# Optimization experiments

Measured on AMD Instinct MI355X. Metric: run time of the kernel, lower is better.

## Reference

```python
import jax, jax.numpy as jnp
import numpy as np

SIGMAS = [0.5, 1.0, 2.0, 4.0, 8.0]
FILTER_SIZE = int(4 * SIGMAS[-1] + 1)  # 33
PAD = int(2 * SIGMAS[-1])              # 16
K1, K2 = 0.01, 0.03
ALPHA = 0.025
COMPENSATION = 20.0
DATA_RANGE = 1.0


def _gauss_2d(size, sigma):
    coords = np.arange(size, dtype=np.float32) - size // 2
    g = np.exp(-coords ** 2 / (2.0 * sigma ** 2))
    g = g / g.sum()
    return np.outer(g, g)


def _build_g_masks():
    # [n_sigmas, 1, 33, 33] OIHW
    masks = np.stack([_gauss_2d(FILTER_SIZE, s)[None] for s in SIGMAS], axis=0)
    return jnp.asarray(masks, dtype=jnp.float32)


def setup_inputs() -> dict:
    key = jax.random.key(0)
    kx, ky = jax.random.split(key)
    x = jax.random.uniform(kx, (16, 1, 512, 512), dtype=jnp.float32)
    y = jax.random.uniform(ky, (16, 1, 512, 512), dtype=jnp.float32)
    return {"x": x, "y": y, "g_masks": _build_g_masks()}


def _conv(t, w):
    # t: [B,1,H,W], w: [O,1,33,33] -> [B,O,H,W] ('same' padding)
    return jax.lax.conv_general_dilated(
        t, w, window_strides=(1, 1), padding=[(PAD, PAD), (PAD, PAD)],
        dimension_numbers=("NCHW", "OIHW", "NCHW"))


def reference(x, y, g_masks):
    C1 = (K1 * DATA_RANGE) ** 2
    C2 = (K2 * DATA_RANGE) ** 2

    mux = _conv(x, g_masks)   # [B,5,H,W]
    muy = _conv(y, g_masks)
    mux2 = mux * mux
    muy2 = muy * muy
    muxy = mux * muy
    sigmax2 = _conv(x * x, g_masks) - mux2
    sigmay2 = _conv(y * y, g_masks) - muy2
    sigmaxy = _conv(x * y, g_masks) - muxy

    luminance = (2.0 * muxy + C1) / (mux2 + muy2 + C1)
    cs = (2.0 * sigmaxy + C2) / (sigmax2 + sigmay2 + C2)

    lM = luminance[:, -1, :, :]          # largest-scale luminance
    PIcs = jnp.prod(cs, axis=1)          # product of contrast-structure over scales
    loss_ms_ssim = 1.0 - lM * PIcs       # [B,H,W]

    loss_l1 = jnp.abs(x - y)             # [B,1,H,W]
    gaussian_l1 = _conv(loss_l1, g_masks[-1:]).mean(axis=1)  # [B,H,W]

    loss_mix = ALPHA * loss_ms_ssim + (1.0 - ALPHA) * gaussian_l1 / DATA_RANGE
    return (COMPENSATION * loss_mix).mean()
```

## Files before the change

kernel.cpp:

```cpp
#include <hip/hip_runtime.h>
#include <hip/hip_bf16.h>

namespace {

constexpr float kAlpha = 0.025f;
constexpr float kC1 = 1.0e-4f;
constexpr float kC2 = 9.0e-4f;

constexpr int MPS = 72;
constexpr int HTS = 72;

typedef __attribute__((ext_vector_type(8))) short short8;
typedef __attribute__((ext_vector_type(4))) float f32x4;

struct __align__(16) Smem {
  union {
    short mp[2][64 * MPS];
    short hbT[4][32 * HTS];
  };
  float red[4];
  int gtab[2][5][48];
};

union Frag {
  int i[4];
  int4 i4;
  short8 s8;
};

__device__ __forceinline__ unsigned f2bf(float f) {
  unsigned u = __float_as_uint(f);
  return (u + 0x7FFFu + ((u >> 16) & 1u)) >> 16;
}
__device__ __forceinline__ unsigned pk(float a, float b) {
  union {
    __hip_bfloat162 h;
    unsigned u;
  } c;
  c.h = __float22bfloat162_rn(make_float2(a, b));
  return c.u;
}
__device__ __forceinline__ float bfl(unsigned u) {
  return __uint_as_float(u << 16);
}
__device__ __forceinline__ float bfh(unsigned u) {
  return __uint_as_float(u & 0xFFFF0000u);
}
__device__ __forceinline__ float frcp(float x) {
  return __builtin_amdgcn_rcpf(x);
}

__device__ __forceinline__ short8 wbuild2(const int* tb, int nt, int kt) {
  Frag u;
#pragma unroll
  for (int j = 0; j < 4; ++j) u.i[j] = tb[16 * kt - 8 * nt + 8 + j];
  return u.s8;
}

__device__ __forceinline__ void load_xy(const Smem& sm, int row, int quad,
                                        Frag fx[2], Frag fy[2]) {
  const short* px = &sm.mp[0][row * MPS + quad * 8];
  const short* py = &sm.mp[1][row * MPS + quad * 8];
  fx[0].i4 = *(const int4*)(px);
  fx[1].i4 = *(const int4*)(px + 32);
  fy[0].i4 = *(const int4*)(py);
  fy[1].i4 = *(const int4*)(py + 32);
}

template <bool USE_WS>
__global__ __launch_bounds__(256, 4) void msssim_l1_kernel(
    const float* __restrict__ x, const float* __restrict__ y,
    const float* __restrict__ gm, float* __restrict__ partial,
    float* __restrict__ out) {
  __shared__ Smem sm;
  const int tid = threadIdx.x;
  const int lane = tid & 63;
  const int w = tid >> 6;
  const int quad = lane >> 4;
  const int l16 = lane & 15;
  const f32x4 kZ = {0.f, 0.f, 0.f, 0.f};

  float corr;
  {
    float traw4 = (lane < 33) ? gm[4 * 1089 + 528 + lane] : 0.f;
    float g = traw4 * rsqrtf(__shfl(traw4, 16, 64));
    float se = g, st = bfl(f2bf(g));
#pragma unroll
    for (int off = 32; off > 0; off >>= 1) {
      se += __shfl_xor(se, off, 64);
      st += __shfl_xor(st, off, 64);
    }
    float r1 = se / st;
    corr = r1 * r1;
  }

  {
    int* gt = &sm.gtab[0][0][0];
    for (int q = tid; q < 480; q += 256) {
      int par = q >= 240;
      int rem = par ? q - 240 : q;
      int s = rem / 48;
      int i = rem - s * 48;
      int t0 = 2 * i + par;
      const float* grow = gm + s * 1089 + 528;
      float rsc = rsqrtf(grow[16]);
      int g0 = t0 - 31, g1 = t0 - 30;
      unsigned lo = (g0 >= 0 && g0 <= 32) ? f2bf(grow[g0] * rsc) : 0u;
      unsigned hi = (g1 >= 0 && g1 <= 32) ? f2bf(grow[g1] * rsc) : 0u;
      gt[q] = (int)(lo | (hi << 16));
    }
  }

  const int D = (quad * 8 - l16 + 31) >> 1;
  const int* gD = &sm.gtab[(l16 & 1) ? 0 : 1][0][0] + D - 8;

  const float* xb = x + blockIdx.z * (512 * 512);
  const float* yb = y + blockIdx.z * (512 * 512);
  const int rb = blockIdx.y * 32 - 16;
  const int cb = blockIdx.x * 32 - 16;
  for (int f = tid; f < 1024; f += 256) {
    int pr = f >> 4;
    int pc = (f & 15) << 2;
    int gr = rb + pr, gc = cb + pc;
    float4 vx = make_float4(0.f, 0.f, 0.f, 0.f);
    float4 vy = vx;
    if (gr >= 0 && gr < 512 && gc >= 0 && gc < 512) {
      vx = *(const float4*)(xb + gr * 512 + gc);
      vy = *(const float4*)(yb + gr * 512 + gc);
    }
    const int base = pr * MPS + pc;
    *(int2*)(&sm.mp[0][base]) =
        make_int2((int)pk(vx.x, vx.y), (int)pk(vx.z, vx.w));
    *(int2*)(&sm.mp[1][base]) =
        make_int2((int)pk(vy.x, vy.y), (int)pk(vy.z, vy.w));
  }
  __syncthreads();

  Frag A[4][2];
  Frag dA[2];
#pragma unroll
  for (int mt = 0; mt < 4; ++mt) {
    Frag fx[2], fy[2];
    load_xy(sm, mt * 16 + l16, quad, fx, fy);
    if (mt == w) {
#pragma unroll
      for (int h = 0; h < 2; ++h)
#pragma unroll
        for (int i = 0; i < 4; ++i) {
          unsigned ux = (unsigned)fx[h].i[i], uy = (unsigned)fy[h].i[i];
          dA[h].i[i] =
              (int)pk(fabsf(bfl(ux) - bfl(uy)), fabsf(bfh(ux) - bfh(uy)));
        }
    }
    if (w == 0) {
      A[mt][0] = fx[0];
      A[mt][1] = fx[1];
    } else if (w == 1) {
      A[mt][0] = fy[0];
      A[mt][1] = fy[1];
    } else {
#pragma unroll
      for (int h = 0; h < 2; ++h)
#pragma unroll
        for (int i = 0; i < 4; ++i) {
          unsigned ux = (unsigned)fx[h].i[i], uy = (unsigned)fy[h].i[i];
          float xl = bfl(ux), xh = bfh(ux), yl = bfl(uy), yh = bfh(uy);
          A[mt][h].i[i] = (w == 2) ? (int)pk(fmaf(xl, xl, yl * yl),
                                            fmaf(xh, xh, yh * yh))
                                   : (int)pk(xl * yl, xh * yh);
        }
    }
  }

  int2 l1h[2];
  {
    const int* tb = gD + 4 * 48;
#pragma unroll
    for (int nt = 0; nt < 2; ++nt) {
      short8 w0 = wbuild2(tb, nt, 0);
      short8 w1 = wbuild2(tb, nt, 1);
      f32x4 acc = __builtin_amdgcn_mfma_f32_16x16x32_bf16(dA[0].s8, w0, kZ, 0,
                                                          0, 0);
      acc = __builtin_amdgcn_mfma_f32_16x16x32_bf16(dA[1].s8, w1, acc, 0, 0,
                                                    0);
      l1h[nt] = make_int2((int)pk(acc[0], acc[1]), (int)pk(acc[2], acc[3]));
    }
  }
  __syncthreads();

  const int mtv = w >> 1, ntv = w & 1;
  f32x4 Pcs = {1.f, 1.f, 1.f, 1.f};
  f32x4 lumP = {0.f, 0.f, 0.f, 0.f};
  f32x4 l1v = {0.f, 0.f, 0.f, 0.f};

#pragma unroll
  for (int s = 0; s < 5; ++s) {
    const int* tb = gD + s * 48;
#pragma unroll
    for (int nt = 0; nt < 2; ++nt) {
      short8 w0 = wbuild2(tb, nt, 0);
      short8 w1 = wbuild2(tb, nt, 1);
#pragma unroll
      for (int mt = 0; mt < 4; ++mt) {
        f32x4 acc = __builtin_amdgcn_mfma_f32_16x16x32_bf16(A[mt][0].s8, w0,
                                                            kZ, 0, 0, 0);
        acc = __builtin_amdgcn_mfma_f32_16x16x32_bf16(A[mt][1].s8, w1, acc, 0,
                                                      0, 0);
        *(int2*)(&sm.hbT[w][(nt * 16 + l16) * HTS + mt * 16 + quad * 4]) =
            make_int2((int)pk(acc[0], acc[1]), (int)pk(acc[2], acc[3]));
      }
    }
    __syncthreads();

    short8 wa0 = wbuild2(tb, mtv, 0);
    short8 wa1 = wbuild2(tb, mtv, 1);
    f32x4 mux, muy, T;
#pragma unroll
    for (int m = 0; m < 4; ++m) {
      const short* bp = &sm.hbT[m][(ntv * 16 + l16) * HTS + quad * 8];
      Frag b0, b1;
      b0.i4 = *(const int4*)(bp);
      b1.i4 = *(const int4*)(bp + 32);
      f32x4 acc =
          __builtin_amdgcn_mfma_f32_16x16x32_bf16(wa0, b0.s8, kZ, 0, 0, 0);
      acc = __builtin_amdgcn_mfma_f32_16x16x32_bf16(wa1, b1.s8, acc, 0, 0, 0);
      if (m == 0) {
        mux = acc;
      } else if (m == 1) {
        muy = acc;
      } else if (m == 2) {
#pragma unroll
        for (int r = 0; r < 4; ++r)
          T[r] = (acc[r] - mux[r] * mux[r]) - muy[r] * muy[r];
      } else {
#pragma unroll
        for (int r = 0; r < 4; ++r) {
          float cs =
              (2.f * (acc[r] - mux[r] * muy[r]) + kC2) * frcp(T[r] + kC2);
          Pcs[r] *= cs;
          if (s == 4)
            lumP[r] = ((2.f * (mux[r] * muy[r]) + kC1) *
                       frcp((mux[r] * mux[r] + muy[r] * muy[r]) + kC1)) *
                      Pcs[r];
        }
      }
    }
    __syncthreads();
  }

  {
    const int* tb = gD + 4 * 48;
#pragma unroll
    for (int nt = 0; nt < 2; ++nt)
      *(int2*)(&sm.hbT[0][(nt * 16 + l16) * HTS + w * 16 + quad * 4]) =
          l1h[nt];
    __syncthreads();

    short8 wa0 = wbuild2(tb, mtv, 0);
    short8 wa1 = wbuild2(tb, mtv, 1);
    const short* bp = &sm.hbT[0][(ntv * 16 + l16) * HTS + quad * 8];
    Frag b0, b1;
    b0.i4 = *(const int4*)(bp);
    b1.i4 = *(const int4*)(bp + 32);
    f32x4 acc =
        __builtin_amdgcn_mfma_f32_16x16x32_bf16(wa0, b0.s8, kZ, 0, 0, 0);
    acc = __builtin_amdgcn_mfma_f32_16x16x32_bf16(wa1, b1.s8, acc, 0, 0, 0);
#pragma unroll
    for (int r = 0; r < 4; ++r) l1v[r] = acc[r] * corr;
  }

  float lsum = 0.f;
#pragma unroll
  for (int r = 0; r < 4; ++r)
    lsum += kAlpha * (1.f - lumP[r]) + (1.f - kAlpha) * l1v[r];
#pragma unroll
  for (int off = 32; off > 0; off >>= 1) lsum += __shfl_down(lsum, off, 64);
  if ((tid & 63) == 0) sm.red[tid >> 6] = lsum;
  __syncthreads();
  if (tid == 0) {
    float t = sm.red[0] + sm.red[1] + sm.red[2] + sm.red[3];
    if (USE_WS) {
      partial[blockIdx.x + (blockIdx.y << 4) + (blockIdx.z << 8)] = t;
    } else {
      atomicAdd(out, t * (20.f / (16.f * 512.f * 512.f)));
    }
  }
}

__global__ __launch_bounds__(256) void msssim_reduce_kernel(
    const float* __restrict__ partial, float* __restrict__ out) {
  const int tid = threadIdx.x;
  float s = 0.f;
#pragma unroll
  for (int i = 0; i < 16; ++i) s += partial[tid + (i << 8)];
#pragma unroll
  for (int off = 32; off > 0; off >>= 1) s += __shfl_xor(s, off, 64);
  __shared__ float red[4];
  if ((tid & 63) == 0) red[tid >> 6] = s;
  __syncthreads();
  if (tid == 0)
    out[0] =
        (red[0] + red[1] + red[2] + red[3]) * (20.f / (16.f * 512.f * 512.f));
}

}

extern "C" void kernel_launch(void* const* d_in, const int* in_sizes, int n_in,
                              void* d_out, int out_size, void* d_ws,
                              size_t ws_size, hipStream_t stream) {
  (void)in_sizes;
  (void)n_in;
  (void)out_size;
  const float* x = (const float*)d_in[0];
  const float* y = (const float*)d_in[1];
  const float* gm = (const float*)d_in[2];
  float* out = (float*)d_out;
  dim3 grid(16, 16, 16);
  if (d_ws != nullptr && ws_size >= 4096 * sizeof(float)) {
    float* partial = (float*)d_ws;
    msssim_l1_kernel<true>
        <<<grid, dim3(256), 0, stream>>>(x, y, gm, partial, out);
    msssim_reduce_kernel<<<1, dim3(256), 0, stream>>>(partial, out);
  } else {
    hipMemsetAsync(out, 0, sizeof(float), stream);
    msssim_l1_kernel<false>
        <<<grid, dim3(256), 0, stream>>>(x, y, gm, nullptr, out);
  }
}
```

Baseline: 126.5 us.

## Enlarge tile to 64x32 output rows with 512-thread blocks sharing halo

Each block now produces a 64-row by 32-column output tile with 8 wavefronts instead of 32x32 with 4. The input halo is loaded once for 96 rows rather than 64 per 32 rows, which cuts redundant halo loads and horizontal-pass MFMA work per output. The second pass is split so each wave handles one 16-row strip. The trade-off is more shared memory and registers per block, which may lower occupancy, and half as many blocks in the grid.

```diff
diff --git a/kernel.cpp b/kernel.cpp
--- a/kernel.cpp
+++ b/kernel.cpp
@@ -8,17 +8,18 @@
 constexpr float kC2 = 9.0e-4f;
 
 constexpr int MPS = 72;
-constexpr int HTS = 72;
+constexpr int HTS = 104;
+constexpr int PRW = 96;
 
 typedef __attribute__((ext_vector_type(8))) short short8;
 typedef __attribute__((ext_vector_type(4))) float f32x4;
 
 struct __align__(16) Smem {
   union {
-    short mp[2][64 * MPS];
+    short mp[2][PRW * MPS];
     short hbT[4][32 * HTS];
   };
-  float red[4];
+  float red[8];
   int gtab[2][5][48];
 };
 
@@ -68,7 +69,7 @@
 }
 
 template <bool USE_WS>
-__global__ __launch_bounds__(256, 4) void msssim_l1_kernel(
+__global__ __launch_bounds__(512, 4) void msssim_l1_kernel(
     const float* __restrict__ x, const float* __restrict__ y,
     const float* __restrict__ gm, float* __restrict__ partial,
     float* __restrict__ out) {
@@ -78,6 +79,13 @@
   const int w = tid >> 6;
   const int quad = lane >> 4;
   const int l16 = lane & 15;
+  const int wmap = w & 3;
+  const int wgrp = w >> 2;
+  const int rt = w >> 1;
+  const int ct = w & 1;
+  const int kb = rt >> 1;
+  const int l1i = w & 3;
+  const bool l1on = l1i < 3;
   const f32x4 kZ = {0.f, 0.f, 0.f, 0.f};
 
   float corr;
@@ -94,21 +102,20 @@
     corr = r1 * r1;
   }
 
-  {
+  if (tid < 480) {
     int* gt = &sm.gtab[0][0][0];
-    for (int q = tid; q < 480; q += 256) {
-      int par = q >= 240;
-      int rem = par ? q - 240 : q;
-      int s = rem / 48;
-      int i = rem - s * 48;
-      int t0 = 2 * i + par;
-      const float* grow = gm + s * 1089 + 528;
-      float rsc = rsqrtf(grow[16]);
-      int g0 = t0 - 31, g1 = t0 - 30;
-      unsigned lo = (g0 >= 0 && g0 <= 32) ? f2bf(grow[g0] * rsc) : 0u;
-      unsigned hi = (g1 >= 0 && g1 <= 32) ? f2bf(grow[g1] * rsc) : 0u;
-      gt[q] = (int)(lo | (hi << 16));
-    }
+    int q = tid;
+    int par = q >= 240;
+    int rem = par ? q - 240 : q;
+    int s = rem / 48;
+    int i = rem - s * 48;
+    int t0 = 2 * i + par;
+    const float* grow = gm + s * 1089 + 528;
+    float rsc = rsqrtf(grow[16]);
+    int g0 = t0 - 31, g1 = t0 - 30;
+    unsigned lo = (g0 >= 0 && g0 <= 32) ? f2bf(grow[g0] * rsc) : 0u;
+    unsigned hi = (g1 >= 0 && g1 <= 32) ? f2bf(grow[g1] * rsc) : 0u;
+    gt[q] = (int)(lo | (hi << 16));
   }
 
   const int D = (quad * 8 - l16 + 31) >> 1;
@@ -116,9 +123,9 @@
 
   const float* xb = x + blockIdx.z * (512 * 512);
   const float* yb = y + blockIdx.z * (512 * 512);
-  const int rb = blockIdx.y * 32 - 16;
+  const int rb = blockIdx.y * 64 - 16;
   const int cb = blockIdx.x * 32 - 16;
-  for (int f = tid; f < 1024; f += 256) {
+  for (int f = tid; f < 1536; f += 512) {
     int pr = f >> 4;
     int pc = (f & 15) << 2;
     int gr = rb + pr, gc = cb + pc;
@@ -136,44 +143,47 @@
   }
   __syncthreads();
 
-  Frag A[4][2];
+  Frag A[3][2];
   Frag dA[2];
-#pragma unroll
-  for (int mt = 0; mt < 4; ++mt) {
+  dA[0].i4 = make_int4(0, 0, 0, 0);
+  dA[1].i4 = make_int4(0, 0, 0, 0);
+#pragma unroll
+  for (int i = 0; i < 3; ++i) {
+    const int mt = 3 * wgrp + i;
     Frag fx[2], fy[2];
     load_xy(sm, mt * 16 + l16, quad, fx, fy);
-    if (mt == w) {
+    if (l1on && i == l1i) {
 #pragma unroll
       for (int h = 0; h < 2; ++h)
 #pragma unroll
-        for (int i = 0; i < 4; ++i) {
-          unsigned ux = (unsigned)fx[h].i[i], uy = (unsigned)fy[h].i[i];
-          dA[h].i[i] =
+        for (int j = 0; j < 4; ++j) {
+          unsigned ux = (unsigned)fx[h].i[j], uy = (unsigned)fy[h].i[j];
+          dA[h].i[j] =
               (int)pk(fabsf(bfl(ux) - bfl(uy)), fabsf(bfh(ux) - bfh(uy)));
         }
     }
-    if (w == 0) {
-      A[mt][0] = fx[0];
-      A[mt][1] = fx[1];
-    } else if (w == 1) {
-      A[mt][0] = fy[0];
-      A[mt][1] = fy[1];
+    if (wmap == 0) {
+      A[i][0] = fx[0];
+      A[i][1] = fx[1];
+    } else if (wmap == 1) {
+      A[i][0] = fy[0];
+      A[i][1] = fy[1];
     } else {
 #pragma unroll
       for (int h = 0; h < 2; ++h)
 #pragma unroll
-        for (int i = 0; i < 4; ++i) {
-          unsigned ux = (unsigned)fx[h].i[i], uy = (unsigned)fy[h].i[i];
+        for (int j = 0; j < 4; ++j) {
+          unsigned ux = (unsigned)fx[h].i[j], uy = (unsigned)fy[h].i[j];
           float xl = bfl(ux), xh = bfh(ux), yl = bfl(uy), yh = bfh(uy);
-          A[mt][h].i[i] = (w == 2) ? (int)pk(fmaf(xl, xl, yl * yl),
-                                            fmaf(xh, xh, yh * yh))
-                                   : (int)pk(xl * yl, xh * yh);
+          A[i][h].i[j] = (wmap == 2) ? (int)pk(fmaf(xl, xl, yl * yl),
+                                              fmaf(xh, xh, yh * yh))
+                                     : (int)pk(xl * yl, xh * yh);
         }
     }
   }
 
-  int2 l1h[2];
-  {
+  int2 l1h[2] = {make_int2(0, 0), make_int2(0, 0)};
+  if (l1on) {
     const int* tb = gD + 4 * 48;
 #pragma unroll
     for (int nt = 0; nt < 2; ++nt) {
@@ -188,7 +198,6 @@
   }
   __syncthreads();
 
-  const int mtv = w >> 1, ntv = w & 1;
   f32x4 Pcs = {1.f, 1.f, 1.f, 1.f};
   f32x4 lumP = {0.f, 0.f, 0.f, 0.f};
   f32x4 l1v = {0.f, 0.f, 0.f, 0.f};
@@ -201,23 +210,24 @@
       short8 w0 = wbuild2(tb, nt, 0);
       short8 w1 = wbuild2(tb, nt, 1);
 #pragma unroll
-      for (int mt = 0; mt < 4; ++mt) {
-        f32x4 acc = __builtin_amdgcn_mfma_f32_16x16x32_bf16(A[mt][0].s8, w0,
+      for (int i = 0; i < 3; ++i) {
+        const int mt = 3 * wgrp + i;
+        f32x4 acc = __builtin_amdgcn_mfma_f32_16x16x32_bf16(A[i][0].s8, w0,
                                                             kZ, 0, 0, 0);
-        acc = __builtin_amdgcn_mfma_f32_16x16x32_bf16(A[mt][1].s8, w1, acc, 0,
+        acc = __builtin_amdgcn_mfma_f32_16x16x32_bf16(A[i][1].s8, w1, acc, 0,
                                                       0, 0);
-        *(int2*)(&sm.hbT[w][(nt * 16 + l16) * HTS + mt * 16 + quad * 4]) =
+        *(int2*)(&sm.hbT[wmap][(nt * 16 + l16) * HTS + mt * 16 + quad * 4]) =
             make_int2((int)pk(acc[0], acc[1]), (int)pk(acc[2], acc[3]));
       }
     }
     __syncthreads();
 
-    short8 wa0 = wbuild2(tb, mtv, 0);
-    short8 wa1 = wbuild2(tb, mtv, 1);
+    short8 wa0 = wbuild2(tb, rt, kb);
+    short8 wa1 = wbuild2(tb, rt, kb + 1);
     f32x4 mux, muy, T;
 #pragma unroll
     for (int m = 0; m < 4; ++m) {
-      const short* bp = &sm.hbT[m][(ntv * 16 + l16) * HTS + quad * 8];
+      const short* bp = &sm.hbT[m][(ct * 16 + l16) * HTS + kb * 32 + quad * 8];
       Frag b0, b1;
       b0.i4 = *(const int4*)(bp);
       b1.i4 = *(const int4*)(bp + 32);
@@ -250,15 +260,17 @@
 
   {
     const int* tb = gD + 4 * 48;
-#pragma unroll
-    for (int nt = 0; nt < 2; ++nt)
-      *(int2*)(&sm.hbT[0][(nt * 16 + l16) * HTS + w * 16 + quad * 4]) =
-          l1h[nt];
+    if (l1on) {
+#pragma unroll
+      for (int nt = 0; nt < 2; ++nt)
+        *(int2*)(&sm.hbT[0][(nt * 16 + l16) * HTS + (3 * wgrp + l1i) * 16 +
+                            quad * 4]) = l1h[nt];
+    }
     __syncthreads();
 
-    short8 wa0 = wbuild2(tb, mtv, 0);
-    short8 wa1 = wbuild2(tb, mtv, 1);
-    const short* bp = &sm.hbT[0][(ntv * 16 + l16) * HTS + quad * 8];
+    short8 wa0 = wbuild2(tb, rt, kb);
+    short8 wa1 = wbuild2(tb, rt, kb + 1);
+    const short* bp = &sm.hbT[0][(ct * 16 + l16) * HTS + kb * 32 + quad * 8];
     Frag b0, b1;
     b0.i4 = *(const int4*)(bp);
     b1.i4 = *(const int4*)(bp + 32);
@@ -278,9 +290,10 @@
   if ((tid & 63) == 0) sm.red[tid >> 6] = lsum;
   __syncthreads();
   if (tid == 0) {
-    float t = sm.red[0] + sm.red[1] + sm.red[2] + sm.red[3];
+    float t = sm.red[0] + sm.red[1] + sm.red[2] + sm.red[3] + sm.red[4] +
+              sm.red[5] + sm.red[6] + sm.red[7];
     if (USE_WS) {
-      partial[blockIdx.x + (blockIdx.y << 4) + (blockIdx.z << 8)] = t;
+      partial[blockIdx.x + (blockIdx.y << 4) + (blockIdx.z << 7)] = t;
     } else {
       atomicAdd(out, t * (20.f / (16.f * 512.f * 512.f)));
     }
@@ -292,7 +305,7 @@
   const int tid = threadIdx.x;
   float s = 0.f;
 #pragma unroll
-  for (int i = 0; i < 16; ++i) s += partial[tid + (i << 8)];
+  for (int i = 0; i < 8; ++i) s += partial[tid + (i << 8)];
 #pragma unroll
   for (int off = 32; off > 0; off >>= 1) s += __shfl_xor(s, off, 64);
   __shared__ float red[4];
@@ -315,15 +328,15 @@
   const float* y = (const float*)d_in[1];
   const float* gm = (const float*)d_in[2];
   float* out = (float*)d_out;
-  dim3 grid(16, 16, 16);
-  if (d_ws != nullptr && ws_size >= 4096 * sizeof(float)) {
+  dim3 grid(16, 8, 16);
+  if (d_ws != nullptr && ws_size >= 2048 * sizeof(float)) {
     float* partial = (float*)d_ws;
     msssim_l1_kernel<true>
-        <<<grid, dim3(256), 0, stream>>>(x, y, gm, partial, out);
+        <<<grid, dim3(512), 0, stream>>>(x, y, gm, partial, out);
     msssim_reduce_kernel<<<1, dim3(256), 0, stream>>>(partial, out);
   } else {
     hipMemsetAsync(out, 0, sizeof(float), stream);
     msssim_l1_kernel<false>
-        <<<grid, dim3(256), 0, stream>>>(x, y, gm, nullptr, out);
-  }
-}
+        <<<grid, dim3(512), 0, stream>>>(x, y, gm, nullptr, out);
+  }
+}
```

Result: no change. 126.8 us (+0.2%).
